# Optimization experiments

Measured on AMD Instinct MI355X. Metric: run time of the kernel, lower is better.

The kernel has to match this reference:

```python
import jax, jax.numpy as jnp
import numpy as np

D_MODEL = 2048
NUM_Q_HEADS = 32
NUM_KV_HEADS = 8
HEAD_DIM = D_MODEL // NUM_Q_HEADS  # 64
NUM_GROUPS = NUM_Q_HEADS // NUM_KV_HEADS  # 4
SCALE = float(np.sqrt(HEAD_DIM))


def setup_inputs() -> dict:
    key = jax.random.key(0)
    ks = jax.random.split(key, 5)
    B, S = 2, 2048
    std = 1.0 / np.sqrt(D_MODEL)
    return {
        "x": jax.random.normal(ks[0], (B, S, D_MODEL), dtype=jnp.float32),
        "W_q": jax.random.normal(ks[1], (D_MODEL, NUM_Q_HEADS * HEAD_DIM), dtype=jnp.float32) * std,
        "W_k": jax.random.normal(ks[2], (D_MODEL, NUM_KV_HEADS * HEAD_DIM), dtype=jnp.float32) * std,
        "W_v": jax.random.normal(ks[3], (D_MODEL, NUM_KV_HEADS * HEAD_DIM), dtype=jnp.float32) * std,
        "W_o": jax.random.normal(ks[4], (D_MODEL, D_MODEL), dtype=jnp.float32) * std,
    }


def reference(x, W_q, W_k, W_v, W_o):
    B, S, _ = x.shape
    # projections; weights stored as (in, out) so y = x @ W
    Q = (x @ W_q).reshape(B, S, NUM_Q_HEADS, HEAD_DIM).transpose(0, 2, 1, 3)   # [B,Hq,S,d]
    K = (x @ W_k).reshape(B, S, NUM_KV_HEADS, HEAD_DIM).transpose(0, 2, 1, 3)  # [B,Hkv,S,d]
    V = (x @ W_v).reshape(B, S, NUM_KV_HEADS, HEAD_DIM).transpose(0, 2, 1, 3)
    # repeat_interleave KV heads across groups (faithful to the original)
    K = jnp.repeat(K, NUM_GROUPS, axis=1)  # [B,Hq,S,d]
    V = jnp.repeat(V, NUM_GROUPS, axis=1)
    scores = jnp.einsum("bhqd,bhkd->bhqk", Q, K) / SCALE  # [B,Hq,S,S]
    attn = jax.nn.softmax(scores, axis=-1)
    out = jnp.einsum("bhqk,bhkd->bhqd", attn, V)  # [B,Hq,S,d]
    out = out.transpose(0, 2, 1, 3).reshape(B, S, D_MODEL)
    return out @ W_o
```

## Files before the change

kernel.cpp:

```cpp
#include <hip/hip_runtime.h>
#include <hip/hip_bf16.h>

#define D_MODEL 2048
#define NQH 32
#define NKVH 8
#define HD 64
#define SEQ 2048
#define BATCH 2
#define MTOT (BATCH * SEQ)

typedef __attribute__((ext_vector_type(8))) short short8;
typedef __attribute__((ext_vector_type(4))) float floatx4;
typedef __attribute__((ext_vector_type(16))) float f32x16;

#define QSCALE 0.18033688011112042f

static __device__ inline unsigned cvtpk(float lo, float hi) {
  unsigned r;
  asm("v_cvt_pk_bf16_f32 %0, %1, %2" : "=v"(r) : "v"(lo), "v"(hi));
  return r;
}
#define PLSWAP(a, b) asm("v_permlane32_swap_b32 %0, %1" : "+v"(a), "+v"(b))

__device__ inline void gload_lds16(const __hip_bfloat16* g, short* lds) {
  __builtin_amdgcn_global_load_lds(
      (const __attribute__((address_space(1))) void*)g,
      (__attribute__((address_space(3))) void*)lds, 16, 0, 0);
}

__global__ __launch_bounds__(256) void convx_k(const float* __restrict__ x,
                                               __hip_bfloat16* __restrict__ xb,
                                               int n4) {
  int i = blockIdx.x * 256 + threadIdx.x;
  int stride = gridDim.x * 256;
  for (; i < n4; i += stride) {
    float4 v = reinterpret_cast<const float4*>(x)[i];
    union { __hip_bfloat16 h[4]; uint2 u; } cv;
    cv.h[0] = __float2bfloat16(v.x);
    cv.h[1] = __float2bfloat16(v.y);
    cv.h[2] = __float2bfloat16(v.z);
    cv.h[3] = __float2bfloat16(v.w);
    reinterpret_cast<uint2*>(xb)[i] = cv.u;
  }
}

__global__ __launch_bounds__(256) void transw_k(const float* __restrict__ W,
                                                __hip_bfloat16* __restrict__ Wt,
                                                int Kd, int Nd) {
  __shared__ float t[32][33];
  int n0 = blockIdx.x * 32, k0 = blockIdx.y * 32;
  int tx = threadIdx.x, ty = threadIdx.y;
#pragma unroll
  for (int j = 0; j < 32; j += 8)
    t[ty + j][tx] = W[(size_t)(k0 + ty + j) * Nd + n0 + tx];
  __syncthreads();
#pragma unroll
  for (int j = 0; j < 32; j += 8)
    Wt[(size_t)(n0 + ty + j) * Kd + k0 + tx] = __float2bfloat16(t[tx][ty + j]);
}

template <int MODE>
__global__ __launch_bounds__(256) void gemm_bt_k(
    const __hip_bfloat16* __restrict__ A,
    const __hip_bfloat16* __restrict__ B0,
    const __hip_bfloat16* __restrict__ B1,
    const __hip_bfloat16* __restrict__ B2,
    float* __restrict__ Cf,
    __hip_bfloat16* __restrict__ O0,
    __hip_bfloat16* __restrict__ O1,
    __hip_bfloat16* __restrict__ O2) {
  constexpr int Kd = D_MODEL;
  __shared__ short As[128 * 32];
  __shared__ short Bs[128 * 32];

  const int tid = threadIdx.x;
  const int m0 = blockIdx.y * 128;
  const int n0 = blockIdx.x * 128;

  const __hip_bfloat16* Bt;
  if (MODE == 0) {
    Bt = B0 + (size_t)n0 * Kd;
  } else {
    if (n0 < 2048) Bt = B0 + (size_t)n0 * Kd;
    else if (n0 < 2560) Bt = B1 + (size_t)(n0 - 2048) * Kd;
    else Bt = B2 + (size_t)(n0 - 2560) * Kd;
  }
  const __hip_bfloat16* Ab = A + (size_t)m0 * Kd;

  const int w = tid >> 6, l = tid & 63;
  const int wr = w >> 1, wc = w & 1;
  const int lc = l & 15, l4 = l >> 4;

  const int srow = w * 32 + (l >> 2);
  const int scol = (l & 3) * 8;
  const __hip_bfloat16* ga = Ab + (size_t)srow * Kd + scol;
  const __hip_bfloat16* gb = Bt + (size_t)srow * Kd + scol;
  short* la0 = &As[(w * 32) * 32];
  short* la1 = &As[(w * 32 + 16) * 32];
  short* lb0 = &Bs[(w * 32) * 32];
  short* lb1 = &Bs[(w * 32 + 16) * 32];

  floatx4 acc[4][4] = {};

  for (int kt = 0; kt < Kd; kt += 32) {
    gload_lds16(ga + kt, la0);
    gload_lds16(ga + (size_t)16 * Kd + kt, la1);
    gload_lds16(gb + kt, lb0);
    gload_lds16(gb + (size_t)16 * Kd + kt, lb1);
    __syncthreads();

    short8 af[4], bf[4];
#pragma unroll
    for (int mi = 0; mi < 4; ++mi)
      af[mi] = *reinterpret_cast<const short8*>(&As[(wr * 64 + mi * 16 + lc) * 32 + l4 * 8]);
#pragma unroll
    for (int ni = 0; ni < 4; ++ni)
      bf[ni] = *reinterpret_cast<const short8*>(&Bs[(wc * 64 + ni * 16 + lc) * 32 + l4 * 8]);
#pragma unroll
    for (int mi = 0; mi < 4; ++mi)
#pragma unroll
      for (int ni = 0; ni < 4; ++ni)
        acc[mi][ni] = __builtin_amdgcn_mfma_f32_16x16x32_bf16(af[mi], bf[ni], acc[mi][ni], 0, 0, 0);
    __syncthreads();
  }

#pragma unroll
  for (int mi = 0; mi < 4; ++mi)
#pragma unroll
    for (int ni = 0; ni < 4; ++ni)
#pragma unroll
      for (int i = 0; i < 4; ++i) {
        int m = m0 + wr * 64 + mi * 16 + l4 * 4 + i;
        int ncol = n0 + wc * 64 + ni * 16 + lc;
        float v = acc[mi][ni][i];
        if (MODE == 0) {
          Cf[(size_t)m * 2048 + ncol] = v;
        } else {
          int bb = m >> 11, s = m & 2047;
          if (ncol < 2048) {
            int hh = ncol >> 6, dd = ncol & 63;
            O0[(((size_t)bb * NQH + hh) * SEQ + s) * HD + dd] = __float2bfloat16(v * QSCALE);
          } else if (ncol < 2560) {
            int c2 = ncol - 2048;
            int hh = c2 >> 6, dd = c2 & 63;
            O1[(((size_t)bb * NKVH + hh) * SEQ + s) * HD + dd] = __float2bfloat16(v);
          } else {
            int c2 = ncol - 2560;
            int hh = c2 >> 6, dd = c2 & 63;
            O2[(((size_t)bb * NKVH + hh) * HD + dd) * SEQ + s] = __float2bfloat16(v);
          }
        }
      }
}

__global__ __launch_bounds__(256, 4) void attn_k(const __hip_bfloat16* __restrict__ Qb,
                                                 const __hip_bfloat16* __restrict__ Kb,
                                                 const __hip_bfloat16* __restrict__ Vtb,
                                                 __hip_bfloat16* __restrict__ Ao) {
  __shared__ short Ks[2][64 * 64];
  __shared__ short Vs[2][64 * 64];
  __shared__ float Ls[4][32];

  const int bid = blockIdx.x;
  const int xcd = bid & 7, j = bid >> 3;
  const int g = xcd * 2 + (j >> 6), wv = j & 63;
  const int b = g >> 3, kh = g & 7;
  const int h = kh * 4 + (wv >> 4), qt = wv & 15;

  const int tid = threadIdx.x, w = tid >> 6, l = tid & 63;
  const int q5 = l & 31, hl = l >> 5;

  const __hip_bfloat16* Qp = Qb + (((size_t)b * NQH + h) * SEQ + qt * 128 + w * 32) * HD;
  const __hip_bfloat16* Kp = Kb + ((size_t)b * NKVH + kh) * SEQ * HD;
  const __hip_bfloat16* Vp = Vtb + ((size_t)b * NKVH + kh) * HD * SEQ;

  short8 qf[4];
#pragma unroll
  for (int ks = 0; ks < 4; ++ks)
    qf[ks] = *reinterpret_cast<const short8*>(Qp + (size_t)q5 * HD + ks * 16 + hl * 8);

  f32x16 acc0 = {}, acc1 = {};
  float lsum = 0.f;

  const int c0 = 2 * w, c1 = 2 * w + 1;
  const __hip_bfloat16* gK0 = Kp + (size_t)l * HD + c0 * 8;
  const __hip_bfloat16* gK1 = Kp + (size_t)l * HD + c1 * 8;
  const __hip_bfloat16* gV0 = Vp + (size_t)l * SEQ + c0 * 8;
  const __hip_bfloat16* gV1 = Vp + (size_t)l * SEQ + c1 * 8;

  gload_lds16(gK0, &Ks[0][c0 * 512]);
  gload_lds16(gK1, &Ks[0][c1 * 512]);
  gload_lds16(gV0, &Vs[0][c0 * 512]);
  gload_lds16(gV1, &Vs[0][c1 * 512]);
  __syncthreads();

  for (int kb = 0; kb < SEQ / 64; ++kb) {
    const short* Kt = Ks[kb & 1];
    const short* Vt = Vs[kb & 1];
    short* Kn = Ks[(kb & 1) ^ 1];
    short* Vn = Vs[(kb & 1) ^ 1];

    short8 kf0[4], kf1[4];
#pragma unroll
    for (int ks = 0; ks < 4; ++ks) {
      kf0[ks] = *reinterpret_cast<const short8*>(Kt + ((ks * 2 + hl) * 64 + q5) * 8);
      kf1[ks] = *reinterpret_cast<const short8*>(Kt + ((ks * 2 + hl) * 64 + 32 + q5) * 8);
    }
    f32x16 st0 = {}, st1 = {};
    __builtin_amdgcn_s_setprio(1);
#pragma unroll
    for (int ks = 0; ks < 4; ++ks) {
      st0 = __builtin_amdgcn_mfma_f32_32x32x16_bf16(kf0[ks], qf[ks], st0, 0, 0, 0);
      st1 = __builtin_amdgcn_mfma_f32_32x32x16_bf16(kf1[ks], qf[ks], st1, 0, 0, 0);
    }
    __builtin_amdgcn_s_setprio(0);

    if (kb < SEQ / 64 - 1) {
      gK0 += 64 * HD; gK1 += 64 * HD; gV0 += 64; gV1 += 64;
      gload_lds16(gK0, &Kn[c0 * 512]);
      gload_lds16(gK1, &Kn[c1 * 512]);
      gload_lds16(gV0, &Vn[c0 * 512]);
      gload_lds16(gV1, &Vn[c1 * 512]);
    }

    float ps = 0.f;
    unsigned u0[8], u1[8];
#pragma unroll
    for (int jj = 0; jj < 8; ++jj) {
      float e0 = exp2f(st0[2 * jj]), e1 = exp2f(st0[2 * jj + 1]);
      float f0 = exp2f(st1[2 * jj]), f1 = exp2f(st1[2 * jj + 1]);
      ps += (e0 + e1) + (f0 + f1);
      u0[jj] = cvtpk(e0, e1);
      u1[jj] = cvtpk(f0, f1);
    }
    lsum += ps;

    short8 vf0[4], vf1[4];
#pragma unroll
    for (int t = 0; t < 4; ++t) {
      vf0[t] = *reinterpret_cast<const short8*>(Vt + ((t * 2 + hl) * 64 + q5) * 8);
      vf1[t] = *reinterpret_cast<const short8*>(Vt + ((t * 2 + hl) * 64 + 32 + q5) * 8);
    }

    PLSWAP(u0[0], u0[2]); PLSWAP(u0[1], u0[3]);
    PLSWAP(u0[4], u0[6]); PLSWAP(u0[5], u0[7]);
    PLSWAP(u1[0], u1[2]); PLSWAP(u1[1], u1[3]);
    PLSWAP(u1[4], u1[6]); PLSWAP(u1[5], u1[7]);

    __builtin_amdgcn_s_setprio(1);
#pragma unroll
    for (int t = 0; t < 4; ++t) {
      union { unsigned w4[4]; short8 s8; } pa;
      pa.w4[0] = (t >> 1 ? u1 : u0)[(t & 1) * 4 + 0];
      pa.w4[1] = (t >> 1 ? u1 : u0)[(t & 1) * 4 + 1];
      pa.w4[2] = (t >> 1 ? u1 : u0)[(t & 1) * 4 + 2];
      pa.w4[3] = (t >> 1 ? u1 : u0)[(t & 1) * 4 + 3];
      acc0 = __builtin_amdgcn_mfma_f32_32x32x16_bf16(pa.s8, vf0[t], acc0, 0, 0, 0);
      acc1 = __builtin_amdgcn_mfma_f32_32x32x16_bf16(pa.s8, vf1[t], acc1, 0, 0, 0);
    }
    __builtin_amdgcn_s_setprio(0);
    __syncthreads();
  }

  {
    float v = lsum;
    v += __shfl_xor(v, 32);
    if (l < 32) Ls[w][l] = v;
  }
  __syncthreads();

  const size_t obase = (size_t)b * SEQ + qt * 128 + w * 32;
  float inv[16];
#pragma unroll
  for (int r = 0; r < 16; ++r)
    inv[r] = 1.0f / Ls[w][(r & 3) + 8 * (r >> 2) + 4 * hl];
#pragma unroll
  for (int r = 0; r < 16; ++r) {
    int q = (r & 3) + 8 * (r >> 2) + 4 * hl;
    Ao[(obase + q) * D_MODEL + h * HD + q5] = __float2bfloat16(acc0[r] * inv[r]);
    Ao[(obase + q) * D_MODEL + h * HD + 32 + q5] = __float2bfloat16(acc1[r] * inv[r]);
  }
}

extern "C" void kernel_launch(void* const* d_in, const int* in_sizes, int n_in,
                              void* d_out, int out_size, void* d_ws, size_t ws_size,
                              hipStream_t stream) {
  const float* x  = (const float*)d_in[0];
  const float* Wq = (const float*)d_in[1];
  const float* Wk = (const float*)d_in[2];
  const float* Wv = (const float*)d_in[3];
  const float* Wo = (const float*)d_in[4];
  float* out = (float*)d_out;

  __hip_bfloat16* p = (__hip_bfloat16*)d_ws;
  __hip_bfloat16* xb  = p;
  __hip_bfloat16* Wqt = xb  + (size_t)MTOT * D_MODEL;
  __hip_bfloat16* Wkt = Wqt + (size_t)D_MODEL * D_MODEL;
  __hip_bfloat16* Wvt = Wkt + (size_t)512 * D_MODEL;
  __hip_bfloat16* Wot = Wvt + (size_t)512 * D_MODEL;
  __hip_bfloat16* Qb  = Wot + (size_t)D_MODEL * D_MODEL;
  __hip_bfloat16* Kb  = Qb  + (size_t)MTOT * D_MODEL;
  __hip_bfloat16* Vtb = Kb  + (size_t)BATCH * NKVH * SEQ * HD;
  __hip_bfloat16* Ab  = Vtb + (size_t)BATCH * NKVH * SEQ * HD;

  convx_k<<<2048, 256, 0, stream>>>(x, xb, MTOT * D_MODEL / 4);
  transw_k<<<dim3(D_MODEL / 32, D_MODEL / 32), dim3(32, 8), 0, stream>>>(Wq, Wqt, D_MODEL, D_MODEL);
  transw_k<<<dim3(512 / 32, D_MODEL / 32), dim3(32, 8), 0, stream>>>(Wk, Wkt, D_MODEL, 512);
  transw_k<<<dim3(512 / 32, D_MODEL / 32), dim3(32, 8), 0, stream>>>(Wv, Wvt, D_MODEL, 512);
  transw_k<<<dim3(D_MODEL / 32, D_MODEL / 32), dim3(32, 8), 0, stream>>>(Wo, Wot, D_MODEL, D_MODEL);

  gemm_bt_k<1><<<dim3(24, MTOT / 128), 256, 0, stream>>>(xb, Wqt, Wkt, Wvt,
                                                         nullptr, Qb, Kb, Vtb);
  attn_k<<<dim3(1024), 256, 0, stream>>>(Qb, Kb, Vtb, Ab);
  gemm_bt_k<0><<<dim3(D_MODEL / 128, MTOT / 128), 256, 0, stream>>>(Ab, Wot, nullptr, nullptr,
                                                                    out, nullptr, nullptr, nullptr);
}
```

Before: 252.4 us.

## Swizzle K/V LDS layout, unroll attention loop by two, use native exp2

Changes the K/V shared-memory tiles from a chunk-major layout to a row-major layout with an XOR swizzle on 16-byte chunks. Both the global-to-LDS copies and the MFMA fragment reads use the swizzled offsets, which is meant to cut LDS bank conflicts. The key-block loop is unrolled by two with fixed buffer offsets, and the next tile's prefetch now starts before the QK MFMAs rather than after them. exp2f is replaced by the raw hardware exp2 builtin, which skips libm's range handling.

```diff
diff --git a/kernel.cpp b/kernel.cpp
--- a/kernel.cpp
+++ b/kernel.cpp
@@ -14,6 +14,12 @@
 typedef __attribute__((ext_vector_type(16))) float f32x16;
 
 #define QSCALE 0.18033688011112042f
+
+#if __has_builtin(__builtin_amdgcn_exp2f)
+#define EXP2(x) __builtin_amdgcn_exp2f(x)
+#else
+#define EXP2(x) exp2f(x)
+#endif
 
 static __device__ inline unsigned cvtpk(float lo, float hi) {
   unsigned r;
@@ -157,8 +163,7 @@
                                                  const __hip_bfloat16* __restrict__ Kb,
                                                  const __hip_bfloat16* __restrict__ Vtb,
                                                  __hip_bfloat16* __restrict__ Ao) {
-  __shared__ short Ks[2][64 * 64];
-  __shared__ short Vs[2][64 * 64];
+  __shared__ short SB[16384];
   __shared__ float Ls[4][32];
 
   const int bid = blockIdx.x;
@@ -182,85 +187,87 @@
   f32x16 acc0 = {}, acc1 = {};
   float lsum = 0.f;
 
-  const int c0 = 2 * w, c1 = 2 * w + 1;
-  const __hip_bfloat16* gK0 = Kp + (size_t)l * HD + c0 * 8;
-  const __hip_bfloat16* gK1 = Kp + (size_t)l * HD + c1 * 8;
-  const __hip_bfloat16* gV0 = Vp + (size_t)l * SEQ + c0 * 8;
-  const __hip_bfloat16* gV1 = Vp + (size_t)l * SEQ + c1 * 8;
-
-  gload_lds16(gK0, &Ks[0][c0 * 512]);
-  gload_lds16(gK1, &Ks[0][c1 * 512]);
-  gload_lds16(gV0, &Vs[0][c0 * 512]);
-  gload_lds16(gV1, &Vs[0][c1 * 512]);
+  const int g0 = 2 * w, g1 = 2 * w + 1;
+  const int r0 = g0 * 8 + (l >> 3), r1 = g1 * 8 + (l >> 3);
+  const int cc0 = (l & 7) ^ ((r0 >> 2) & 7);
+  const int cc1 = (l & 7) ^ ((r1 >> 2) & 7);
+  const __hip_bfloat16* sK0 = Kp + (size_t)r0 * HD + cc0 * 8;
+  const __hip_bfloat16* sK1 = Kp + (size_t)r1 * HD + cc1 * 8;
+  const __hip_bfloat16* sV0 = Vp + (size_t)r0 * SEQ + cc0 * 8;
+  const __hip_bfloat16* sV1 = Vp + (size_t)r1 * SEQ + cc1 * 8;
+
+#define STAGE(B)                                     \
+  do {                                               \
+    gload_lds16(sK0, &SB[(B) + g0 * 512]);           \
+    gload_lds16(sK1, &SB[(B) + g1 * 512]);           \
+    gload_lds16(sV0, &SB[(B) + 4096 + g0 * 512]);    \
+    gload_lds16(sV1, &SB[(B) + 4096 + g1 * 512]);    \
+    sK0 += 64 * HD; sK1 += 64 * HD; sV0 += 64; sV1 += 64; \
+  } while (0)
+
+  const int sw = (q5 >> 2) & 7;
+  int fo[4];
+#pragma unroll
+  for (int jj = 0; jj < 4; ++jj)
+    fo[jj] = q5 * 64 + (((jj * 2 + hl) ^ sw) * 8);
+
+  STAGE(0);
   __syncthreads();
 
-  for (int kb = 0; kb < SEQ / 64; ++kb) {
-    const short* Kt = Ks[kb & 1];
-    const short* Vt = Vs[kb & 1];
-    short* Kn = Ks[(kb & 1) ^ 1];
-    short* Vn = Vs[(kb & 1) ^ 1];
-
-    short8 kf0[4], kf1[4];
-#pragma unroll
-    for (int ks = 0; ks < 4; ++ks) {
-      kf0[ks] = *reinterpret_cast<const short8*>(Kt + ((ks * 2 + hl) * 64 + q5) * 8);
-      kf1[ks] = *reinterpret_cast<const short8*>(Kt + ((ks * 2 + hl) * 64 + 32 + q5) * 8);
-    }
-    f32x16 st0 = {}, st1 = {};
-    __builtin_amdgcn_s_setprio(1);
-#pragma unroll
-    for (int ks = 0; ks < 4; ++ks) {
-      st0 = __builtin_amdgcn_mfma_f32_32x32x16_bf16(kf0[ks], qf[ks], st0, 0, 0, 0);
-      st1 = __builtin_amdgcn_mfma_f32_32x32x16_bf16(kf1[ks], qf[ks], st1, 0, 0, 0);
-    }
-    __builtin_amdgcn_s_setprio(0);
-
-    if (kb < SEQ / 64 - 1) {
-      gK0 += 64 * HD; gK1 += 64 * HD; gV0 += 64; gV1 += 64;
-      gload_lds16(gK0, &Kn[c0 * 512]);
-      gload_lds16(gK1, &Kn[c1 * 512]);
-      gload_lds16(gV0, &Vn[c0 * 512]);
-      gload_lds16(gV1, &Vn[c1 * 512]);
-    }
-
-    float ps = 0.f;
-    unsigned u0[8], u1[8];
-#pragma unroll
-    for (int jj = 0; jj < 8; ++jj) {
-      float e0 = exp2f(st0[2 * jj]), e1 = exp2f(st0[2 * jj + 1]);
-      float f0 = exp2f(st1[2 * jj]), f1 = exp2f(st1[2 * jj + 1]);
-      ps += (e0 + e1) + (f0 + f1);
-      u0[jj] = cvtpk(e0, e1);
-      u1[jj] = cvtpk(f0, f1);
-    }
-    lsum += ps;
-
-    short8 vf0[4], vf1[4];
-#pragma unroll
-    for (int t = 0; t < 4; ++t) {
-      vf0[t] = *reinterpret_cast<const short8*>(Vt + ((t * 2 + hl) * 64 + q5) * 8);
-      vf1[t] = *reinterpret_cast<const short8*>(Vt + ((t * 2 + hl) * 64 + 32 + q5) * 8);
-    }
-
-    PLSWAP(u0[0], u0[2]); PLSWAP(u0[1], u0[3]);
-    PLSWAP(u0[4], u0[6]); PLSWAP(u0[5], u0[7]);
-    PLSWAP(u1[0], u1[2]); PLSWAP(u1[1], u1[3]);
-    PLSWAP(u1[4], u1[6]); PLSWAP(u1[5], u1[7]);
-
-    __builtin_amdgcn_s_setprio(1);
-#pragma unroll
-    for (int t = 0; t < 4; ++t) {
-      union { unsigned w4[4]; short8 s8; } pa;
-      pa.w4[0] = (t >> 1 ? u1 : u0)[(t & 1) * 4 + 0];
-      pa.w4[1] = (t >> 1 ? u1 : u0)[(t & 1) * 4 + 1];
-      pa.w4[2] = (t >> 1 ? u1 : u0)[(t & 1) * 4 + 2];
-      pa.w4[3] = (t >> 1 ? u1 : u0)[(t & 1) * 4 + 3];
-      acc0 = __builtin_amdgcn_mfma_f32_32x32x16_bf16(pa.s8, vf0[t], acc0, 0, 0, 0);
-      acc1 = __builtin_amdgcn_mfma_f32_32x32x16_bf16(pa.s8, vf1[t], acc1, 0, 0, 0);
-    }
-    __builtin_amdgcn_s_setprio(0);
-    __syncthreads();
-  }
+#define BODY(KB, RB, SBF)                                                       \
+  do {                                                                          \
+    if ((KB) + 1 < SEQ / 64) STAGE(SBF);                                        \
+    short8 kf0[4], kf1[4];                                                      \
+    _Pragma("unroll") for (int ks = 0; ks < 4; ++ks) {                          \
+      kf0[ks] = *reinterpret_cast<const short8*>(&SB[(RB) + fo[ks]]);           \
+      kf1[ks] = *reinterpret_cast<const short8*>(&SB[(RB) + fo[ks] + 2048]);    \
+    }                                                                           \
+    f32x16 st0 = {}, st1 = {};                                                  \
+    __builtin_amdgcn_s_setprio(1);                                              \
+    _Pragma("unroll") for (int ks = 0; ks < 4; ++ks) {                          \
+      st0 = __builtin_amdgcn_mfma_f32_32x32x16_bf16(kf0[ks], qf[ks], st0, 0, 0, 0); \
+      st1 = __builtin_amdgcn_mfma_f32_32x32x16_bf16(kf1[ks], qf[ks], st1, 0, 0, 0); \
+    }                                                                           \
+    __builtin_amdgcn_s_setprio(0);                                              \
+    float ps = 0.f;                                                             \
+    unsigned u0[8], u1[8];                                                      \
+    _Pragma("unroll") for (int jj = 0; jj < 8; ++jj) {                          \
+      float e0 = EXP2(st0[2 * jj]), e1 = EXP2(st0[2 * jj + 1]);                 \
+      float f0 = EXP2(st1[2 * jj]), f1 = EXP2(st1[2 * jj + 1]);                 \
+      ps += (e0 + e1) + (f0 + f1);                                              \
+      u0[jj] = cvtpk(e0, e1);                                                   \
+      u1[jj] = cvtpk(f0, f1);                                                   \
+    }                                                                           \
+    lsum += ps;                                                                 \
+    short8 vf0[4], vf1[4];                                                      \
+    _Pragma("unroll") for (int t = 0; t < 4; ++t) {                             \
+      vf0[t] = *reinterpret_cast<const short8*>(&SB[(RB) + fo[t] + 4096]);      \
+      vf1[t] = *reinterpret_cast<const short8*>(&SB[(RB) + fo[t] + 6144]);      \
+    }                                                                           \
+    PLSWAP(u0[0], u0[2]); PLSWAP(u0[1], u0[3]);                                 \
+    PLSWAP(u0[4], u0[6]); PLSWAP(u0[5], u0[7]);                                 \
+    PLSWAP(u1[0], u1[2]); PLSWAP(u1[1], u1[3]);                                 \
+    PLSWAP(u1[4], u1[6]); PLSWAP(u1[5], u1[7]);                                 \
+    __builtin_amdgcn_s_setprio(1);                                              \
+    _Pragma("unroll") for (int t = 0; t < 4; ++t) {                             \
+      union { unsigned w4[4]; short8 s8; } pa;                                  \
+      pa.w4[0] = (t >> 1 ? u1 : u0)[(t & 1) * 4 + 0];                           \
+      pa.w4[1] = (t >> 1 ? u1 : u0)[(t & 1) * 4 + 1];                           \
+      pa.w4[2] = (t >> 1 ? u1 : u0)[(t & 1) * 4 + 2];                           \
+      pa.w4[3] = (t >> 1 ? u1 : u0)[(t & 1) * 4 + 3];                           \
+      acc0 = __builtin_amdgcn_mfma_f32_32x32x16_bf16(pa.s8, vf0[t], acc0, 0, 0, 0); \
+      acc1 = __builtin_amdgcn_mfma_f32_32x32x16_bf16(pa.s8, vf1[t], acc1, 0, 0, 0); \
+    }                                                                           \
+    __builtin_amdgcn_s_setprio(0);                                              \
+    __syncthreads();                                                            \
+  } while (0)
+
+  for (int kb = 0; kb < SEQ / 64; kb += 2) {
+    BODY(kb, 0, 8192);
+    BODY(kb + 1, 8192, 0);
+  }
+#undef BODY
+#undef STAGE
 
   {
     float v = lsum;
```

Measured after the change: 272.9 us. 1.08x slower.

## Swizzle K/V LDS layout for coalesced loads, prefetch earlier, use native exp2

Applied to the files above, without the earlier changes.

Changes the global-to-LDS staging so each lane loads contiguous 16-byte chunks of eight rows with an XOR swizzle on the column chunk, and adjusts the LDS fragment reads to use the matching swizzled offsets. The intent is more coalesced global reads and fewer LDS bank conflicts. The next tile's prefetch now starts at the top of each iteration rather than after the QK MFMAs, giving more overlap. exp2f is replaced with the hardware exp2 builtin when it is available, which drops the range handling in exp2f.

```diff
diff --git a/kernel.cpp b/kernel.cpp
--- a/kernel.cpp
+++ b/kernel.cpp
@@ -14,6 +14,12 @@
 typedef __attribute__((ext_vector_type(16))) float f32x16;
 
 #define QSCALE 0.18033688011112042f
+
+#if __has_builtin(__builtin_amdgcn_exp2f)
+#define EXP2(x) __builtin_amdgcn_exp2f(x)
+#else
+#define EXP2(x) exp2f(x)
+#endif
 
 static __device__ inline unsigned cvtpk(float lo, float hi) {
   unsigned r;
@@ -182,29 +188,44 @@
   f32x16 acc0 = {}, acc1 = {};
   float lsum = 0.f;
 
-  const int c0 = 2 * w, c1 = 2 * w + 1;
-  const __hip_bfloat16* gK0 = Kp + (size_t)l * HD + c0 * 8;
-  const __hip_bfloat16* gK1 = Kp + (size_t)l * HD + c1 * 8;
-  const __hip_bfloat16* gV0 = Vp + (size_t)l * SEQ + c0 * 8;
-  const __hip_bfloat16* gV1 = Vp + (size_t)l * SEQ + c1 * 8;
-
-  gload_lds16(gK0, &Ks[0][c0 * 512]);
-  gload_lds16(gK1, &Ks[0][c1 * 512]);
-  gload_lds16(gV0, &Vs[0][c0 * 512]);
-  gload_lds16(gV1, &Vs[0][c1 * 512]);
+  const int rg = l >> 3;
+  const int cc = (l & 7) ^ (rg & 7);
+  const __hip_bfloat16* sK = Kp + (size_t)(16 * w + rg) * HD + cc * 8;
+  const __hip_bfloat16* sV = Vp + (size_t)(16 * w + rg) * SEQ + cc * 8;
+
+  int fo[4];
+#pragma unroll
+  for (int jj = 0; jj < 4; ++jj)
+    fo[jj] = q5 * 64 + (((jj * 2 + hl) ^ (q5 & 7)) * 8);
+
+  gload_lds16(sK, &Ks[0][1024 * w]);
+  gload_lds16(sK + 8 * HD, &Ks[0][1024 * w + 512]);
+  gload_lds16(sV, &Vs[0][1024 * w]);
+  gload_lds16(sV + 8 * (size_t)SEQ, &Vs[0][1024 * w + 512]);
+  sK += 64 * HD;
+  sV += 64;
   __syncthreads();
 
   for (int kb = 0; kb < SEQ / 64; ++kb) {
     const short* Kt = Ks[kb & 1];
     const short* Vt = Vs[kb & 1];
-    short* Kn = Ks[(kb & 1) ^ 1];
-    short* Vn = Vs[(kb & 1) ^ 1];
+
+    if (kb + 1 < SEQ / 64) {
+      short* Kn = Ks[(kb & 1) ^ 1];
+      short* Vn = Vs[(kb & 1) ^ 1];
+      gload_lds16(sK, &Kn[1024 * w]);
+      gload_lds16(sK + 8 * HD, &Kn[1024 * w + 512]);
+      gload_lds16(sV, &Vn[1024 * w]);
+      gload_lds16(sV + 8 * (size_t)SEQ, &Vn[1024 * w + 512]);
+      sK += 64 * HD;
+      sV += 64;
+    }
 
     short8 kf0[4], kf1[4];
 #pragma unroll
     for (int ks = 0; ks < 4; ++ks) {
-      kf0[ks] = *reinterpret_cast<const short8*>(Kt + ((ks * 2 + hl) * 64 + q5) * 8);
-      kf1[ks] = *reinterpret_cast<const short8*>(Kt + ((ks * 2 + hl) * 64 + 32 + q5) * 8);
+      kf0[ks] = *reinterpret_cast<const short8*>(&Kt[fo[ks]]);
+      kf1[ks] = *reinterpret_cast<const short8*>(&Kt[fo[ks] + 2048]);
     }
     f32x16 st0 = {}, st1 = {};
     __builtin_amdgcn_s_setprio(1);
@@ -215,20 +236,12 @@
     }
     __builtin_amdgcn_s_setprio(0);
 
-    if (kb < SEQ / 64 - 1) {
-      gK0 += 64 * HD; gK1 += 64 * HD; gV0 += 64; gV1 += 64;
-      gload_lds16(gK0, &Kn[c0 * 512]);
-      gload_lds16(gK1, &Kn[c1 * 512]);
-      gload_lds16(gV0, &Vn[c0 * 512]);
-      gload_lds16(gV1, &Vn[c1 * 512]);
-    }
-
     float ps = 0.f;
     unsigned u0[8], u1[8];
 #pragma unroll
     for (int jj = 0; jj < 8; ++jj) {
-      float e0 = exp2f(st0[2 * jj]), e1 = exp2f(st0[2 * jj + 1]);
-      float f0 = exp2f(st1[2 * jj]), f1 = exp2f(st1[2 * jj + 1]);
+      float e0 = EXP2(st0[2 * jj]), e1 = EXP2(st0[2 * jj + 1]);
+      float f0 = EXP2(st1[2 * jj]), f1 = EXP2(st1[2 * jj + 1]);
       ps += (e0 + e1) + (f0 + f1);
       u0[jj] = cvtpk(e0, e1);
       u1[jj] = cvtpk(f0, f1);
@@ -238,8 +251,8 @@
     short8 vf0[4], vf1[4];
 #pragma unroll
     for (int t = 0; t < 4; ++t) {
-      vf0[t] = *reinterpret_cast<const short8*>(Vt + ((t * 2 + hl) * 64 + q5) * 8);
-      vf1[t] = *reinterpret_cast<const short8*>(Vt + ((t * 2 + hl) * 64 + 32 + q5) * 8);
+      vf0[t] = *reinterpret_cast<const short8*>(&Vt[fo[t]]);
+      vf1[t] = *reinterpret_cast<const short8*>(&Vt[fo[t] + 2048]);
     }
 
     PLSWAP(u0[0], u0[2]); PLSWAP(u0[1], u0[3]);
```

After: 232.0 us. 1.09x faster.
